# Kernel optimization log

Hardware: AMD Instinct MI355X
Metric: run time of the kernel (lower is better)

The kernel has to match this reference:

```python
import jax, jax.numpy as jnp
import numpy as np

B, M, N, C = 8192, 16, 256, 64


def setup_inputs() -> dict:
    key = jax.random.key(0)
    k1, k2 = jax.random.split(key)
    inputs = jax.random.normal(k1, (B, M, C), dtype=jnp.float32)
    codebook = jax.random.normal(k2, (M, N, C), dtype=jnp.float32)
    return {"inputs": inputs, "codebook": codebook}


def reference(inputs, codebook):
    # inputs: [B, M, C]; codebook: [M, N, C]
    # (avoids materializing the torch [B, M, N, C] broadcast difference)
    x2 = jnp.sum(inputs * inputs, axis=-1)[:, :, None]          # [B, M, 1]
    c2 = jnp.sum(codebook * codebook, axis=-1)[None, :, :]      # [1, M, N]
    xc = jnp.einsum('bmc,mnc->bmn', inputs, codebook)           # [B, M, N]
    dist = x2 - 2.0 * xc + c2                                   # [B, M, N]
    idx = jnp.argmin(dist, axis=-1)                             # [B, M] int
    m_idx = jnp.arange(codebook.shape[0])[None, :]              # [1, M]
    codes = codebook[m_idx, idx]                                # [B, M, C]
    return codes, idx
```

## Files before the change

kernel.cpp:

```cpp
#include <hip/hip_runtime.h>
#include <hip/hip_bf16.h>
#include <float.h>


#define BQ 8192
#define MQ 16
#define NQ 256
#define CQ 64

typedef short  shortx8 __attribute__((ext_vector_type(8)));
typedef float  f32x4   __attribute__((ext_vector_type(4)));

__device__ __forceinline__ unsigned short f2bf(float f, float& rem) {
    __hip_bfloat16 h = __float2bfloat16(f);
    rem = f - __bfloat162float(h);
    return __builtin_bit_cast(unsigned short, h);
}

__global__ __launch_bounds__(256) void fq_prep_kernel(
        const float* __restrict__ codebook,
        unsigned short* __restrict__ cb3f,
        float* __restrict__ c2) {
    const int t  = blockIdx.x * 256 + threadIdx.x;
    const int kc = t & 7;
    const int e  = t >> 3;
    const int m  = e >> 8, n = e & 255;
    const int nt = n >> 4, col = n & 15;
    const int h = kc >> 2, quad = kc & 3;

    const float* src = codebook + (size_t)e * CQ + kc * 8;
    const float4 va = *(const float4*)src;
    const float4 vb = *(const float4*)(src + 4);
    const float el[8] = {va.x, va.y, va.z, va.w, vb.x, vb.y, vb.z, vb.w};

    float s = 0.0f;
    #pragma unroll
    for (int u = 0; u < 8; ++u) s = fmaf(el[u], el[u], s);
    s += __shfl_xor(s, 1, 64);
    s += __shfl_xor(s, 2, 64);
    s += __shfl_xor(s, 4, 64);
    if (kc == 0) c2[e] = s;

    uint p0[4], p1[4], p2[4];
    #pragma unroll
    for (int u = 0; u < 4; ++u) {
        float r1, r2, d;
        const float a = el[2 * u], b = el[2 * u + 1];
        const unsigned short a0 = f2bf(a, r1);
        const unsigned short a1 = f2bf(r1, r2);
        const unsigned short a2 = f2bf(r2, d);
        const unsigned short b0 = f2bf(b, r1);
        const unsigned short b1 = f2bf(r1, r2);
        const unsigned short b2 = f2bf(r2, d);
        p0[u] = (uint)a0 | ((uint)b0 << 16);
        p1[u] = (uint)a1 | ((uint)b1 << 16);
        p2[u] = (uint)a2 | ((uint)b2 << 16);
    }
    const int lane_f = quad * 16 + col;
    #pragma unroll
    for (int j = 0; j < 3; ++j) {
        const uint* p = (j == 0) ? p0 : (j == 1) ? p1 : p2;
        const int frag = ((m * 3 + j) * 2 + h) * 16 + nt;
        uint4* dst = (uint4*)(cb3f + ((size_t)frag * 64 + lane_f) * 8);
        *dst = make_uint4(p[0], p[1], p[2], p[3]);
    }
}

__global__ __launch_bounds__(256, 3) void fq_main_kernel(
        const float* __restrict__ inputs,
        const float* __restrict__ codebook,
        const unsigned short* __restrict__ cb3f,
        const float* __restrict__ c2,
        float* __restrict__ out_codes,
        float* __restrict__ out_idx) {
    const int m    = blockIdx.y;
    const int row0 = blockIdx.x * 64;
    const int w    = threadIdx.x >> 6;
    const int lane = threadIdx.x & 63;
    const int quad = lane >> 4;
    const int col  = lane & 15;
    const int rg   = w & 1;
    const int chh  = w >> 1;

    __shared__ float sxf[64][68];
    __shared__ float s_c2[NQ];
    __shared__ float s_wb[2][64];
    __shared__ int   s_wi[2][64];
    __shared__ int   s_win[64];

    s_c2[threadIdx.x] = c2[m * NQ + threadIdx.x];

    #pragma unroll
    for (int i = 0; i < 4; ++i) {
        const int f = threadIdx.x + 256 * i;
        const int r = f >> 4;
        const int c = (f & 15) * 4;
        const float4 v = *(const float4*)(
            inputs + ((size_t)(row0 + r) * MQ + m) * CQ + c);
        *(float4*)&sxf[r][c] = v;
    }
    __syncthreads();

    shortx8 afr[3][2][2];
    #pragma unroll
    for (int rt = 0; rt < 2; ++rt)
        #pragma unroll
        for (int h = 0; h < 2; ++h) {
            const float* xp = &sxf[rg * 32 + rt * 16 + col][h * 32 + quad * 8];
            const float4 va = *(const float4*)xp;
            const float4 vb = *(const float4*)(xp + 4);
            const float el[8] = {va.x, va.y, va.z, va.w, vb.x, vb.y, vb.z, vb.w};
            shortx8 a0, a1, a2;
            #pragma unroll
            for (int u = 0; u < 8; ++u) {
                float r1, r2, d;
                a0[u] = (short)f2bf(el[u], r1);
                a1[u] = (short)f2bf(r1, r2);
                a2[u] = (short)f2bf(r2, d);
            }
            afr[0][rt][h] = a0; afr[1][rt][h] = a1; afr[2][rt][h] = a2;
        }

    f32x4 acc[2][8];
    #pragma unroll
    for (int rt = 0; rt < 2; ++rt)
        #pragma unroll
        for (int nt = 0; nt < 8; ++nt)
            acc[rt][nt] = (f32x4){0.f, 0.f, 0.f, 0.f};

    #pragma unroll
    for (int h = 0; h < 2; ++h) {
        #pragma unroll
        for (int j = 0; j < 3; ++j) {
            const int frag0 = ((m * 3 + j) * 2 + h) * 16 + chh * 8;
            const unsigned short* bp =
                cb3f + ((size_t)frag0 * 64 + lane) * 8;
            shortx8 bfr[8];
            #pragma unroll
            for (int nt = 0; nt < 8; ++nt)
                bfr[nt] = *(const shortx8*)(bp + (size_t)nt * 64 * 8);
            #pragma unroll
            for (int i = 0; i <= 2 - j; ++i) {
                #pragma unroll
                for (int nt = 0; nt < 8; ++nt) {
                    acc[0][nt] = __builtin_amdgcn_mfma_f32_16x16x32_bf16(
                        afr[i][0][h], bfr[nt], acc[0][nt], 0, 0, 0);
                    acc[1][nt] = __builtin_amdgcn_mfma_f32_16x16x32_bf16(
                        afr[i][1][h], bfr[nt], acc[1][nt], 0, 0, 0);
                }
            }
        }
    }

    float c2r[8];
    #pragma unroll
    for (int nt = 0; nt < 8; ++nt)
        c2r[nt] = s_c2[chh * 128 + nt * 16 + col];

    #pragma unroll
    for (int rt = 0; rt < 2; ++rt) {
        #pragma unroll
        for (int reg = 0; reg < 4; ++reg) {
            float bd = FLT_MAX; int bi = 0;
            #pragma unroll
            for (int nt = 0; nt < 8; ++nt) {
                const float d = fmaf(-2.0f, acc[rt][nt][reg], c2r[nt]);
                if (d < bd) { bd = d; bi = chh * 128 + nt * 16 + col; }
            }
            #pragma unroll
            for (int mask = 1; mask <= 8; mask <<= 1) {
                const float od = __shfl_xor(bd, mask, 64);
                const int   oi = __shfl_xor(bi, mask, 64);
                if (od < bd || (od == bd && oi < bi)) { bd = od; bi = oi; }
            }
            if (col == 0) {
                const int r = rg * 32 + rt * 16 + quad * 4 + reg;
                s_wb[chh][r] = bd;
                s_wi[chh][r] = bi;
            }
        }
    }
    __syncthreads();

    if (w == 0) {
        float bd = s_wb[0][lane]; int bi = s_wi[0][lane];
        const float od = s_wb[1][lane]; const int oi = s_wi[1][lane];
        if (od < bd || (od == bd && oi < bi)) { bd = od; bi = oi; }
        s_win[lane] = bi;
        out_idx[(size_t)(row0 + lane) * MQ + m] = (float)bi;
    }
    __syncthreads();

    const float* cbm = codebook + (size_t)m * NQ * CQ;
    #pragma unroll 4
    for (int jj = 0; jj < 16; ++jj) {
        const int r  = w * 16 + jj;
        const int bn = s_win[r];
        out_codes[((size_t)(row0 + r) * MQ + m) * CQ + lane] =
            cbm[(size_t)bn * CQ + lane];
    }
}

extern "C" void kernel_launch(void* const* d_in, const int* in_sizes, int n_in,
                              void* d_out, int out_size, void* d_ws, size_t ws_size,
                              hipStream_t stream) {
    const float* inputs   = (const float*)d_in[0];
    const float* codebook = (const float*)d_in[1];
    float* out_codes = (float*)d_out;
    float* out_idx   = (float*)d_out + (size_t)BQ * MQ * CQ;
    float*          c2   = (float*)d_ws;
    unsigned short* cb3f = (unsigned short*)(c2 + MQ * NQ);

    fq_prep_kernel<<<dim3(128), 256, 0, stream>>>(codebook, cb3f, c2);

    fq_main_kernel<<<dim3(BQ / 64, MQ), 256, 0, stream>>>(
        inputs, codebook, cb3f, c2, out_codes, out_idx);
}
```

Before: 121.0 us.

## Process multiple row tiles per block with async LDS prefetch ring

The main kernel now loops over four 64-row tiles per block. Input tiles are staged into a triple-buffered, XOR-swizzled LDS ring via direct global-to-LDS loads, so the next tiles' loads overlap the current tile's MFMA work. The grid shrinks by four and the prep kernel's block size is halved. The intent is to hide input load latency and amortize per-block setup, at the cost of fewer blocks and lower parallelism across CUs.

Result: slower. 191.7 us (+58.4%).

```diff
diff --git a/kernel.cpp b/kernel.cpp
--- a/kernel.cpp
+++ b/kernel.cpp
@@ -7,6 +7,7 @@
 #define MQ 16
 #define NQ 256
 #define CQ 64
+#define TILES 4
 
 typedef short  shortx8 __attribute__((ext_vector_type(8)));
 typedef float  f32x4   __attribute__((ext_vector_type(4)));
@@ -17,11 +18,11 @@
     return __builtin_bit_cast(unsigned short, h);
 }
 
-__global__ __launch_bounds__(256) void fq_prep_kernel(
+__global__ __launch_bounds__(128) void fq_prep_kernel(
         const float* __restrict__ codebook,
         unsigned short* __restrict__ cb3f,
         float* __restrict__ c2) {
-    const int t  = blockIdx.x * 256 + threadIdx.x;
+    const int t  = blockIdx.x * 128 + threadIdx.x;
     const int kc = t & 7;
     const int e  = t >> 3;
     const int m  = e >> 8, n = e & 255;
@@ -66,6 +67,22 @@
     }
 }
 
+__device__ __forceinline__ void fq_stage(const float* __restrict__ inputs,
+        int row0, int m, float* lds_base, int w, int lane) {
+    #pragma unroll
+    for (int i = 0; i < 4; ++i) {
+        const int blk = i * 4 + w;
+        const int f   = (blk << 6) + lane;
+        const int r   = f >> 4;
+        const int c   = (f & 15) ^ (r & 7);
+        const float* src = inputs + ((size_t)(row0 + r) * MQ + m) * CQ + (c << 2);
+        __builtin_amdgcn_global_load_lds(
+            (const __attribute__((address_space(1))) void*)src,
+            (__attribute__((address_space(3))) void*)(lds_base + (blk << 8)),
+            16, 0, 0);
+    }
+}
+
 __global__ __launch_bounds__(256, 3) void fq_main_kernel(
         const float* __restrict__ inputs,
         const float* __restrict__ codebook,
@@ -74,15 +91,15 @@
         float* __restrict__ out_codes,
         float* __restrict__ out_idx) {
     const int m    = blockIdx.y;
-    const int row0 = blockIdx.x * 64;
     const int w    = threadIdx.x >> 6;
     const int lane = threadIdx.x & 63;
     const int quad = lane >> 4;
     const int col  = lane & 15;
     const int rg   = w & 1;
     const int chh  = w >> 1;
-
-    __shared__ float sxf[64][68];
+    const int rowB = blockIdx.x * (TILES * 64);
+
+    __shared__ float sx[3][64][64];
     __shared__ float s_c2[NQ];
     __shared__ float s_wb[2][64];
     __shared__ int   s_wi[2][64];
@@ -90,114 +107,119 @@
 
     s_c2[threadIdx.x] = c2[m * NQ + threadIdx.x];
 
-    #pragma unroll
-    for (int i = 0; i < 4; ++i) {
-        const int f = threadIdx.x + 256 * i;
-        const int r = f >> 4;
-        const int c = (f & 15) * 4;
-        const float4 v = *(const float4*)(
-            inputs + ((size_t)(row0 + r) * MQ + m) * CQ + c);
-        *(float4*)&sxf[r][c] = v;
-    }
-    __syncthreads();
-
-    shortx8 afr[3][2][2];
-    #pragma unroll
-    for (int rt = 0; rt < 2; ++rt)
+    fq_stage(inputs, rowB,      m, &sx[0][0][0], w, lane);
+    fq_stage(inputs, rowB + 64, m, &sx[1][0][0], w, lane);
+
+    #pragma unroll 1
+    for (int t = 0; t < TILES; ++t) {
+        const int row0 = rowB + (t << 6);
+        const float* sxb = &sx[t % 3][0][0];
+        __syncthreads();
+
+        if (t + 2 < TILES)
+            fq_stage(inputs, row0 + 128, m, &sx[(t + 2) % 3][0][0], w, lane);
+
+        shortx8 afr[3][2][2];
+        #pragma unroll
+        for (int rt = 0; rt < 2; ++rt)
+            #pragma unroll
+            for (int h = 0; h < 2; ++h) {
+                const int rr = rg * 32 + rt * 16 + col;
+                const int p0 = (h * 8 + quad * 2) ^ (rr & 7);
+                const float* rowp = sxb + rr * 64;
+                const float4 va = *(const float4*)(rowp + (p0 << 2));
+                const float4 vb = *(const float4*)(rowp + ((p0 ^ 1) << 2));
+                const float el[8] = {va.x, va.y, va.z, va.w,
+                                     vb.x, vb.y, vb.z, vb.w};
+                shortx8 a0, a1, a2;
+                #pragma unroll
+                for (int u = 0; u < 8; ++u) {
+                    float r1, r2, d;
+                    a0[u] = (short)f2bf(el[u], r1);
+                    a1[u] = (short)f2bf(r1, r2);
+                    a2[u] = (short)f2bf(r2, d);
+                }
+                afr[0][rt][h] = a0; afr[1][rt][h] = a1; afr[2][rt][h] = a2;
+            }
+
+        f32x4 acc[2][8];
+        #pragma unroll
+        for (int rt = 0; rt < 2; ++rt)
+            #pragma unroll
+            for (int nt = 0; nt < 8; ++nt)
+                acc[rt][nt] = (f32x4){0.f, 0.f, 0.f, 0.f};
+
         #pragma unroll
         for (int h = 0; h < 2; ++h) {
-            const float* xp = &sxf[rg * 32 + rt * 16 + col][h * 32 + quad * 8];
-            const float4 va = *(const float4*)xp;
-            const float4 vb = *(const float4*)(xp + 4);
-            const float el[8] = {va.x, va.y, va.z, va.w, vb.x, vb.y, vb.z, vb.w};
-            shortx8 a0, a1, a2;
-            #pragma unroll
-            for (int u = 0; u < 8; ++u) {
-                float r1, r2, d;
-                a0[u] = (short)f2bf(el[u], r1);
-                a1[u] = (short)f2bf(r1, r2);
-                a2[u] = (short)f2bf(r2, d);
+            #pragma unroll
+            for (int j = 0; j < 3; ++j) {
+                const int frag0 = ((m * 3 + j) * 2 + h) * 16 + chh * 8;
+                const unsigned short* bp =
+                    cb3f + ((size_t)frag0 * 64 + lane) * 8;
+                shortx8 bfr[8];
+                #pragma unroll
+                for (int nt = 0; nt < 8; ++nt)
+                    bfr[nt] = *(const shortx8*)(bp + (size_t)nt * 64 * 8);
+                #pragma unroll
+                for (int i = 0; i <= 2 - j; ++i) {
+                    #pragma unroll
+                    for (int nt = 0; nt < 8; ++nt) {
+                        acc[0][nt] = __builtin_amdgcn_mfma_f32_16x16x32_bf16(
+                            afr[i][0][h], bfr[nt], acc[0][nt], 0, 0, 0);
+                        acc[1][nt] = __builtin_amdgcn_mfma_f32_16x16x32_bf16(
+                            afr[i][1][h], bfr[nt], acc[1][nt], 0, 0, 0);
+                    }
+                }
             }
-            afr[0][rt][h] = a0; afr[1][rt][h] = a1; afr[2][rt][h] = a2;
-        }
-
-    f32x4 acc[2][8];
-    #pragma unroll
-    for (int rt = 0; rt < 2; ++rt)
+        }
+
+        float c2r[8];
         #pragma unroll
         for (int nt = 0; nt < 8; ++nt)
-            acc[rt][nt] = (f32x4){0.f, 0.f, 0.f, 0.f};
-
-    #pragma unroll
-    for (int h = 0; h < 2; ++h) {
-        #pragma unroll
-        for (int j = 0; j < 3; ++j) {
-            const int frag0 = ((m * 3 + j) * 2 + h) * 16 + chh * 8;
-            const unsigned short* bp =
-                cb3f + ((size_t)frag0 * 64 + lane) * 8;
-            shortx8 bfr[8];
-            #pragma unroll
-            for (int nt = 0; nt < 8; ++nt)
-                bfr[nt] = *(const shortx8*)(bp + (size_t)nt * 64 * 8);
-            #pragma unroll
-            for (int i = 0; i <= 2 - j; ++i) {
+            c2r[nt] = s_c2[chh * 128 + nt * 16 + col];
+
+        #pragma unroll
+        for (int rt = 0; rt < 2; ++rt) {
+            #pragma unroll
+            for (int reg = 0; reg < 4; ++reg) {
+                float bd = FLT_MAX; int bi = 0;
                 #pragma unroll
                 for (int nt = 0; nt < 8; ++nt) {
-                    acc[0][nt] = __builtin_amdgcn_mfma_f32_16x16x32_bf16(
-                        afr[i][0][h], bfr[nt], acc[0][nt], 0, 0, 0);
-                    acc[1][nt] = __builtin_amdgcn_mfma_f32_16x16x32_bf16(
-                        afr[i][1][h], bfr[nt], acc[1][nt], 0, 0, 0);
+                    const float d = fmaf(-2.0f, acc[rt][nt][reg], c2r[nt]);
+                    if (d < bd) { bd = d; bi = chh * 128 + nt * 16 + col; }
+                }
+                #pragma unroll
+                for (int mask = 1; mask <= 8; mask <<= 1) {
+                    const float od = __shfl_xor(bd, mask, 64);
+                    const int   oi = __shfl_xor(bi, mask, 64);
+                    if (od < bd || (od == bd && oi < bi)) { bd = od; bi = oi; }
+                }
+                if (col == 0) {
+                    const int r = rg * 32 + rt * 16 + quad * 4 + reg;
+                    s_wb[chh][r] = bd;
+                    s_wi[chh][r] = bi;
                 }
             }
         }
-    }
-
-    float c2r[8];
-    #pragma unroll
-    for (int nt = 0; nt < 8; ++nt)
-        c2r[nt] = s_c2[chh * 128 + nt * 16 + col];
-
-    #pragma unroll
-    for (int rt = 0; rt < 2; ++rt) {
-        #pragma unroll
-        for (int reg = 0; reg < 4; ++reg) {
-            float bd = FLT_MAX; int bi = 0;
-            #pragma unroll
-            for (int nt = 0; nt < 8; ++nt) {
-                const float d = fmaf(-2.0f, acc[rt][nt][reg], c2r[nt]);
-                if (d < bd) { bd = d; bi = chh * 128 + nt * 16 + col; }
-            }
-            #pragma unroll
-            for (int mask = 1; mask <= 8; mask <<= 1) {
-                const float od = __shfl_xor(bd, mask, 64);
-                const int   oi = __shfl_xor(bi, mask, 64);
-                if (od < bd || (od == bd && oi < bi)) { bd = od; bi = oi; }
-            }
-            if (col == 0) {
-                const int r = rg * 32 + rt * 16 + quad * 4 + reg;
-                s_wb[chh][r] = bd;
-                s_wi[chh][r] = bi;
-            }
-        }
-    }
-    __syncthreads();
-
-    if (w == 0) {
-        float bd = s_wb[0][lane]; int bi = s_wi[0][lane];
-        const float od = s_wb[1][lane]; const int oi = s_wi[1][lane];
-        if (od < bd || (od == bd && oi < bi)) { bd = od; bi = oi; }
-        s_win[lane] = bi;
-        out_idx[(size_t)(row0 + lane) * MQ + m] = (float)bi;
-    }
-    __syncthreads();
-
-    const float* cbm = codebook + (size_t)m * NQ * CQ;
-    #pragma unroll 4
-    for (int jj = 0; jj < 16; ++jj) {
-        const int r  = w * 16 + jj;
-        const int bn = s_win[r];
-        out_codes[((size_t)(row0 + r) * MQ + m) * CQ + lane] =
-            cbm[(size_t)bn * CQ + lane];
+        __syncthreads();
+
+        if (w == 0) {
+            float bd = s_wb[0][lane]; int bi = s_wi[0][lane];
+            const float od = s_wb[1][lane]; const int oi = s_wi[1][lane];
+            if (od < bd || (od == bd && oi < bi)) { bd = od; bi = oi; }
+            s_win[lane] = bi;
+            out_idx[(size_t)(row0 + lane) * MQ + m] = (float)bi;
+        }
+        __syncthreads();
+
+        const float* cbm = codebook + (size_t)m * NQ * CQ;
+        #pragma unroll 4
+        for (int jj = 0; jj < 16; ++jj) {
+            const int r  = w * 16 + jj;
+            const int bn = s_win[r];
+            out_codes[((size_t)(row0 + r) * MQ + m) * CQ + lane] =
+                cbm[(size_t)bn * CQ + lane];
+        }
     }
 }
 
@@ -211,8 +233,8 @@
     float*          c2   = (float*)d_ws;
     unsigned short* cb3f = (unsigned short*)(c2 + MQ * NQ);
 
-    fq_prep_kernel<<<dim3(128), 256, 0, stream>>>(codebook, cb3f, c2);
-
-    fq_main_kernel<<<dim3(BQ / 64, MQ), 256, 0, stream>>>(
+    fq_prep_kernel<<<dim3(256), 128, 0, stream>>>(codebook, cb3f, c2);
+
+    fq_main_kernel<<<dim3(BQ / 64 / TILES, MQ), 256, 0, stream>>>(
         inputs, codebook, cb3f, c2, out_codes, out_idx);
 }
```

## Process two row tiles per block with register prefetch of next input tile

Applied to the files above, without the earlier changes.

Each main-kernel block now handles two 64-row tiles instead of one. It prefetches the next tile's inputs into registers while running MFMA on the current tile, and double-buffers the shared-memory staging. The first codebook fragment load is hoisted ahead of the A-fragment conversion. The prep kernel is relaunched with 128-thread blocks. This halves the grid to amortize per-block setup and hide global load latency, but it raises LDS use and register pressure, which may lower occupancy under the 3-blocks-per-CU launch bound.

New measurement: 127.3 us. 1.05x slower.

```diff
diff --git a/kernel.cpp b/kernel.cpp
--- a/kernel.cpp
+++ b/kernel.cpp
@@ -7,6 +7,7 @@
 #define MQ 16
 #define NQ 256
 #define CQ 64
+#define TILES 2
 
 typedef short  shortx8 __attribute__((ext_vector_type(8)));
 typedef float  f32x4   __attribute__((ext_vector_type(4)));
@@ -17,11 +18,11 @@
     return __builtin_bit_cast(unsigned short, h);
 }
 
-__global__ __launch_bounds__(256) void fq_prep_kernel(
+__global__ __launch_bounds__(128) void fq_prep_kernel(
         const float* __restrict__ codebook,
         unsigned short* __restrict__ cb3f,
         float* __restrict__ c2) {
-    const int t  = blockIdx.x * 256 + threadIdx.x;
+    const int t  = blockIdx.x * 128 + threadIdx.x;
     const int kc = t & 7;
     const int e  = t >> 3;
     const int m  = e >> 8, n = e & 255;
@@ -74,15 +75,15 @@
         float* __restrict__ out_codes,
         float* __restrict__ out_idx) {
     const int m    = blockIdx.y;
-    const int row0 = blockIdx.x * 64;
     const int w    = threadIdx.x >> 6;
     const int lane = threadIdx.x & 63;
     const int quad = lane >> 4;
     const int col  = lane & 15;
     const int rg   = w & 1;
     const int chh  = w >> 1;
-
-    __shared__ float sxf[64][68];
+    const int rowB = blockIdx.x * (TILES * 64);
+
+    __shared__ float sx[2][64][68];
     __shared__ float s_c2[NQ];
     __shared__ float s_wb[2][64];
     __shared__ int   s_wi[2][64];
@@ -96,108 +97,147 @@
         const int r = f >> 4;
         const int c = (f & 15) * 4;
         const float4 v = *(const float4*)(
-            inputs + ((size_t)(row0 + r) * MQ + m) * CQ + c);
-        *(float4*)&sxf[r][c] = v;
+            inputs + ((size_t)(rowB + r) * MQ + m) * CQ + c);
+        *(float4*)&sx[0][r][c] = v;
     }
     __syncthreads();
 
-    shortx8 afr[3][2][2];
-    #pragma unroll
-    for (int rt = 0; rt < 2; ++rt)
-        #pragma unroll
-        for (int h = 0; h < 2; ++h) {
-            const float* xp = &sxf[rg * 32 + rt * 16 + col][h * 32 + quad * 8];
-            const float4 va = *(const float4*)xp;
-            const float4 vb = *(const float4*)(xp + 4);
-            const float el[8] = {va.x, va.y, va.z, va.w, vb.x, vb.y, vb.z, vb.w};
-            shortx8 a0, a1, a2;
-            #pragma unroll
-            for (int u = 0; u < 8; ++u) {
-                float r1, r2, d;
-                a0[u] = (short)f2bf(el[u], r1);
-                a1[u] = (short)f2bf(r1, r2);
-                a2[u] = (short)f2bf(r2, d);
-            }
-            afr[0][rt][h] = a0; afr[1][rt][h] = a1; afr[2][rt][h] = a2;
-        }
-
-    f32x4 acc[2][8];
-    #pragma unroll
-    for (int rt = 0; rt < 2; ++rt)
-        #pragma unroll
-        for (int nt = 0; nt < 8; ++nt)
-            acc[rt][nt] = (f32x4){0.f, 0.f, 0.f, 0.f};
-
-    #pragma unroll
-    for (int h = 0; h < 2; ++h) {
-        #pragma unroll
-        for (int j = 0; j < 3; ++j) {
-            const int frag0 = ((m * 3 + j) * 2 + h) * 16 + chh * 8;
-            const unsigned short* bp =
-                cb3f + ((size_t)frag0 * 64 + lane) * 8;
-            shortx8 bfr[8];
+    #pragma unroll
+    for (int t = 0; t < TILES; ++t) {
+        const int row0 = rowB + t * 64;
+        const float (*sxf)[68] = sx[t & 1];
+
+        float4 pf[4];
+        if (t + 1 < TILES) {
+            #pragma unroll
+            for (int i = 0; i < 4; ++i) {
+                const int f = threadIdx.x + 256 * i;
+                const int r = f >> 4;
+                const int c = (f & 15) * 4;
+                pf[i] = *(const float4*)(
+                    inputs + ((size_t)(row0 + 64 + r) * MQ + m) * CQ + c);
+            }
+        }
+
+        shortx8 bfr[8];
+        {
+            const int frag0 = (m * 3 * 2) * 16 + chh * 8;
+            const unsigned short* bp = cb3f + ((size_t)frag0 * 64 + lane) * 8;
             #pragma unroll
             for (int nt = 0; nt < 8; ++nt)
                 bfr[nt] = *(const shortx8*)(bp + (size_t)nt * 64 * 8);
-            #pragma unroll
-            for (int i = 0; i <= 2 - j; ++i) {
+        }
+
+        shortx8 afr[3][2][2];
+        #pragma unroll
+        for (int rt = 0; rt < 2; ++rt)
+            #pragma unroll
+            for (int h = 0; h < 2; ++h) {
+                const float* xp = &sxf[rg * 32 + rt * 16 + col][h * 32 + quad * 8];
+                const float4 va = *(const float4*)xp;
+                const float4 vb = *(const float4*)(xp + 4);
+                const float el[8] = {va.x, va.y, va.z, va.w,
+                                     vb.x, vb.y, vb.z, vb.w};
+                shortx8 a0, a1, a2;
+                #pragma unroll
+                for (int u = 0; u < 8; ++u) {
+                    float r1, r2, d;
+                    a0[u] = (short)f2bf(el[u], r1);
+                    a1[u] = (short)f2bf(r1, r2);
+                    a2[u] = (short)f2bf(r2, d);
+                }
+                afr[0][rt][h] = a0; afr[1][rt][h] = a1; afr[2][rt][h] = a2;
+            }
+
+        f32x4 acc[2][8];
+        #pragma unroll
+        for (int rt = 0; rt < 2; ++rt)
+            #pragma unroll
+            for (int nt = 0; nt < 8; ++nt)
+                acc[rt][nt] = (f32x4){0.f, 0.f, 0.f, 0.f};
+
+        #pragma unroll
+        for (int h = 0; h < 2; ++h) {
+            #pragma unroll
+            for (int j = 0; j < 3; ++j) {
+                if (!(h == 0 && j == 0)) {
+                    const int frag0 = ((m * 3 + j) * 2 + h) * 16 + chh * 8;
+                    const unsigned short* bp =
+                        cb3f + ((size_t)frag0 * 64 + lane) * 8;
+                    #pragma unroll
+                    for (int nt = 0; nt < 8; ++nt)
+                        bfr[nt] = *(const shortx8*)(bp + (size_t)nt * 64 * 8);
+                }
+                #pragma unroll
+                for (int i = 0; i <= 2 - j; ++i) {
+                    #pragma unroll
+                    for (int nt = 0; nt < 8; ++nt) {
+                        acc[0][nt] = __builtin_amdgcn_mfma_f32_16x16x32_bf16(
+                            afr[i][0][h], bfr[nt], acc[0][nt], 0, 0, 0);
+                        acc[1][nt] = __builtin_amdgcn_mfma_f32_16x16x32_bf16(
+                            afr[i][1][h], bfr[nt], acc[1][nt], 0, 0, 0);
+                    }
+                }
+            }
+        }
+
+        if (t + 1 < TILES) {
+            #pragma unroll
+            for (int i = 0; i < 4; ++i) {
+                const int f = threadIdx.x + 256 * i;
+                const int r = f >> 4;
+                const int c = (f & 15) * 4;
+                *(float4*)&sx[(t + 1) & 1][r][c] = pf[i];
+            }
+        }
+
+        float c2r[8];
+        #pragma unroll
+        for (int nt = 0; nt < 8; ++nt)
+            c2r[nt] = s_c2[chh * 128 + nt * 16 + col];
+
+        #pragma unroll
+        for (int rt = 0; rt < 2; ++rt) {
+            #pragma unroll
+            for (int reg = 0; reg < 4; ++reg) {
+                float bd = FLT_MAX; int bi = 0;
                 #pragma unroll
                 for (int nt = 0; nt < 8; ++nt) {
-                    acc[0][nt] = __builtin_amdgcn_mfma_f32_16x16x32_bf16(
-                        afr[i][0][h], bfr[nt], acc[0][nt], 0, 0, 0);
-                    acc[1][nt] = __builtin_amdgcn_mfma_f32_16x16x32_bf16(
-                        afr[i][1][h], bfr[nt], acc[1][nt], 0, 0, 0);
-                }
-            }
-        }
-    }
-
-    float c2r[8];
-    #pragma unroll
-    for (int nt = 0; nt < 8; ++nt)
-        c2r[nt] = s_c2[chh * 128 + nt * 16 + col];
-
-    #pragma unroll
-    for (int rt = 0; rt < 2; ++rt) {
-        #pragma unroll
-        for (int reg = 0; reg < 4; ++reg) {
-            float bd = FLT_MAX; int bi = 0;
-            #pragma unroll
-            for (int nt = 0; nt < 8; ++nt) {
-                const float d = fmaf(-2.0f, acc[rt][nt][reg], c2r[nt]);
-                if (d < bd) { bd = d; bi = chh * 128 + nt * 16 + col; }
-            }
-            #pragma unroll
-            for (int mask = 1; mask <= 8; mask <<= 1) {
-                const float od = __shfl_xor(bd, mask, 64);
-                const int   oi = __shfl_xor(bi, mask, 64);
-                if (od < bd || (od == bd && oi < bi)) { bd = od; bi = oi; }
-            }
-            if (col == 0) {
-                const int r = rg * 32 + rt * 16 + quad * 4 + reg;
-                s_wb[chh][r] = bd;
-                s_wi[chh][r] = bi;
-            }
-        }
-    }
-    __syncthreads();
-
-    if (w == 0) {
-        float bd = s_wb[0][lane]; int bi = s_wi[0][lane];
-        const float od = s_wb[1][lane]; const int oi = s_wi[1][lane];
-        if (od < bd || (od == bd && oi < bi)) { bd = od; bi = oi; }
-        s_win[lane] = bi;
-        out_idx[(size_t)(row0 + lane) * MQ + m] = (float)bi;
-    }
-    __syncthreads();
-
-    const float* cbm = codebook + (size_t)m * NQ * CQ;
-    #pragma unroll 4
-    for (int jj = 0; jj < 16; ++jj) {
-        const int r  = w * 16 + jj;
-        const int bn = s_win[r];
-        out_codes[((size_t)(row0 + r) * MQ + m) * CQ + lane] =
-            cbm[(size_t)bn * CQ + lane];
+                    const float d = fmaf(-2.0f, acc[rt][nt][reg], c2r[nt]);
+                    if (d < bd) { bd = d; bi = chh * 128 + nt * 16 + col; }
+                }
+                #pragma unroll
+                for (int mask = 1; mask <= 8; mask <<= 1) {
+                    const float od = __shfl_xor(bd, mask, 64);
+                    const int   oi = __shfl_xor(bi, mask, 64);
+                    if (od < bd || (od == bd && oi < bi)) { bd = od; bi = oi; }
+                }
+                if (col == 0) {
+                    const int r = rg * 32 + rt * 16 + quad * 4 + reg;
+                    s_wb[chh][r] = bd;
+                    s_wi[chh][r] = bi;
+                }
+            }
+        }
+        __syncthreads();
+
+        if (w == 0) {
+            float bd = s_wb[0][lane]; int bi = s_wi[0][lane];
+            const float od = s_wb[1][lane]; const int oi = s_wi[1][lane];
+            if (od < bd || (od == bd && oi < bi)) { bd = od; bi = oi; }
+            s_win[lane] = bi;
+            out_idx[(size_t)(row0 + lane) * MQ + m] = (float)bi;
+        }
+        __syncthreads();
+
+        const float* cbm = codebook + (size_t)m * NQ * CQ;
+        #pragma unroll 4
+        for (int jj = 0; jj < 16; ++jj) {
+            const int r  = w * 16 + jj;
+            const int bn = s_win[r];
+            out_codes[((size_t)(row0 + r) * MQ + m) * CQ + lane] =
+                cbm[(size_t)bn * CQ + lane];
+        }
     }
 }
 
@@ -211,8 +251,8 @@
     float*          c2   = (float*)d_ws;
     unsigned short* cb3f = (unsigned short*)(c2 + MQ * NQ);
 
-    fq_prep_kernel<<<dim3(128), 256, 0, stream>>>(codebook, cb3f, c2);
-
-    fq_main_kernel<<<dim3(BQ / 64, MQ), 256, 0, stream>>>(
+    fq_prep_kernel<<<dim3(256), 128, 0, stream>>>(codebook, cb3f, c2);
+
+    fq_main_kernel<<<dim3(BQ / 64 / TILES, MQ), 256, 0, stream>>>(
         inputs, codebook, cb3f, c2, out_codes, out_idx);
 }
```
